# Optimization experiments

Measured on AMD Instinct MI355X. Metric: run time of the kernel, lower is better.

The kernel has to match this reference:

```python
import jax, jax.numpy as jnp
import numpy as np

B, S, P, D = 32, 512, 512, 768

def setup_inputs() -> dict:
    key = jax.random.key(0)
    k1, k2 = jax.random.split(key)
    inputs = jax.random.normal(k1, (B, S, D), dtype=jnp.float32)
    prototypes = jax.random.normal(k2, (P, D), dtype=jnp.float32)
    return {"inputs": inputs, "prototypes": prototypes}

def reference(inputs, prototypes):
    # Squared Euclidean distance from every token vector to every prototype:
    # but the cross term is a GEMM and the huge [B,S,P,D] intermediate is never built).
    x_sq = jnp.sum(inputs * inputs, axis=-1, keepdims=True)          # [B, S, 1]
    p_sq = jnp.sum(prototypes * prototypes, axis=-1)                 # [P]
    cross = jnp.einsum('bsd,pd->bsp', inputs, prototypes)            # [B, S, P]
    distances = x_sq + p_sq[None, None, :] - 2.0 * cross             # [B, S, P]
    return (distances, prototypes)
```

## Files before the change

kernel.cpp:

```cpp
#include <hip/hip_runtime.h>
#include <hip/hip_bf16.h>


#define M_TOK 16384
#define N_PROT 512
#define K_DIM 768

typedef __attribute__((ext_vector_type(4))) float f32x4;
typedef __attribute__((ext_vector_type(8))) short bf16x8;

typedef const __attribute__((address_space(1))) unsigned int g_uint;
typedef __attribute__((address_space(3))) unsigned int l_uint;

__device__ inline unsigned short f2bf(float f) {
    unsigned int u = __float_as_uint(f);
    u += 0x7fffu + ((u >> 16) & 1u);
    return (unsigned short)(u >> 16);
}

__global__ __launch_bounds__(256) void prep_kernel(
    const float* __restrict__ x, const float* __restrict__ p,
    unsigned short* __restrict__ a_bf, unsigned short* __restrict__ b_bf,
    float* __restrict__ x_sq, float* __restrict__ p_sq,
    float* __restrict__ proto_out)
{
    const int row  = blockIdx.x * 4 + (threadIdx.x >> 6);
    const int lane = threadIdx.x & 63;

    const float4* src4;
    unsigned short* dst;
    float4* pout4 = nullptr;
    if (row < M_TOK) {
        src4 = (const float4*)(x + (size_t)row * K_DIM);
        dst  = a_bf + (size_t)row * K_DIM;
    } else {
        const int r = row - M_TOK;
        src4  = (const float4*)(p + (size_t)r * K_DIM);
        dst   = b_bf + (size_t)r * K_DIM;
        pout4 = (float4*)(proto_out + (size_t)r * K_DIM);
    }

    float ssum = 0.0f;
#pragma unroll
    for (int j = 0; j < 3; ++j) {
        const int idx = lane + j * 64;
        float4 v = src4[idx];
        ssum += v.x * v.x + v.y * v.y + v.z * v.z + v.w * v.w;
        ushort4 b;
        b.x = f2bf(v.x); b.y = f2bf(v.y); b.z = f2bf(v.z); b.w = f2bf(v.w);
        ((ushort4*)dst)[idx] = b;
        if (pout4) pout4[idx] = v;
    }

#pragma unroll
    for (int off = 32; off > 0; off >>= 1) ssum += __shfl_down(ssum, off);
    if (lane == 0) {
        if (row < M_TOK) x_sq[row] = ssum;
        else             p_sq[row - M_TOK] = ssum;
    }
}

__global__ __launch_bounds__(256) void gemm_kernel(
    const unsigned short* __restrict__ A,
    const unsigned short* __restrict__ Bt,
    const float* __restrict__ x_sq, const float* __restrict__ p_sq,
    float* __restrict__ out)
{
    __shared__ unsigned short lds_a[128 * 32];
    __shared__ unsigned short lds_b[128 * 32];

    const int tid  = threadIdx.x;
    const int wave = tid >> 6;
    const int lane = tid & 63;
    const int bm = blockIdx.y << 7;
    const int bn = blockIdx.x << 7;
    const int wm = (wave >> 1) << 6;
    const int wn = (wave & 1) << 6;
    const int quad = lane >> 4;
    const int l16  = lane & 15;

    const int srow = wave * 32;
    const int lrow = lane >> 2;
    const int lcol = (lane & 3) * 8;

    const f32x4 zero = {0.0f, 0.0f, 0.0f, 0.0f};
    f32x4 acc[4][4];
#pragma unroll
    for (int mt = 0; mt < 4; ++mt)
#pragma unroll
        for (int nt = 0; nt < 4; ++nt) acc[mt][nt] = zero;

    for (int k0 = 0; k0 < K_DIM; k0 += 32) {
        __syncthreads();
#pragma unroll
        for (int i = 0; i < 2; ++i) {
            const unsigned short* ga =
                A + (size_t)(bm + srow + i * 16 + lrow) * K_DIM + k0 + lcol;
            __builtin_amdgcn_global_load_lds((g_uint*)ga,
                (l_uint*)&lds_a[(srow + i * 16) * 32], 16, 0, 0);
            const unsigned short* gb =
                Bt + (size_t)(bn + srow + i * 16 + lrow) * K_DIM + k0 + lcol;
            __builtin_amdgcn_global_load_lds((g_uint*)gb,
                (l_uint*)&lds_b[(srow + i * 16) * 32], 16, 0, 0);
        }
        __syncthreads();

        bf16x8 af[4], bfr[4];
#pragma unroll
        for (int mt = 0; mt < 4; ++mt)
            af[mt] = *(const bf16x8*)&lds_a[(wm + mt * 16 + l16) * 32 + quad * 8];
#pragma unroll
        for (int nt = 0; nt < 4; ++nt)
            bfr[nt] = *(const bf16x8*)&lds_b[(wn + nt * 16 + l16) * 32 + quad * 8];

#pragma unroll
        for (int mt = 0; mt < 4; ++mt)
#pragma unroll
            for (int nt = 0; nt < 4; ++nt)
                acc[mt][nt] = __builtin_amdgcn_mfma_f32_16x16x32_bf16(
                    af[mt], bfr[nt], acc[mt][nt], 0, 0, 0);
    }

    float ps[4];
#pragma unroll
    for (int nt = 0; nt < 4; ++nt) ps[nt] = p_sq[bn + wn + nt * 16 + l16];

#pragma unroll
    for (int mt = 0; mt < 4; ++mt) {
#pragma unroll
        for (int i = 0; i < 4; ++i) {
            const int gr = bm + wm + mt * 16 + quad * 4 + i;
            const float xs = x_sq[gr];
            float* orow = out + (size_t)gr * N_PROT + bn + wn + l16;
#pragma unroll
            for (int nt = 0; nt < 4; ++nt)
                orow[nt * 16] = xs + ps[nt] - 2.0f * acc[mt][nt][i];
        }
    }
}

extern "C" void kernel_launch(void* const* d_in, const int* in_sizes, int n_in,
                              void* d_out, int out_size, void* d_ws, size_t ws_size,
                              hipStream_t stream) {
    const float* inputs = (const float*)d_in[0];
    const float* protos = (const float*)d_in[1];
    float* out = (float*)d_out;

    char* ws = (char*)d_ws;
    unsigned short* a_bf = (unsigned short*)ws;
    unsigned short* b_bf = (unsigned short*)(ws + 25165824);
    float* x_sq = (float*)(ws + 25165824 + 786432);
    float* p_sq = (float*)(ws + 25165824 + 786432 + 65536);
    float* proto_out = out + (size_t)M_TOK * N_PROT;

    prep_kernel<<<4224, 256, 0, stream>>>(inputs, protos, a_bf, b_bf, x_sq, p_sq, proto_out);

    dim3 grid(N_PROT / 128, M_TOK / 128);
    gemm_kernel<<<grid, 256, 0, stream>>>(a_bf, b_bf, x_sq, p_sq, out);
}
```

Measured before the change: 117.1 us.

## Fuse bf16 conversion and norm computation into the GEMM kernel

Removes the separate prep kernel that converted inputs and prototypes to bf16 and computed squared norms. The GEMM kernel now loads fp32 tiles directly, computes the row norms while loading, converts to bf16 into LDS, and also writes the prototype passthrough from the first block row. The K tile grows from 32 to 64, and the launch bounds now ask for two blocks per CU. This avoids the bf16 round trip through workspace and one launch, but each block now reads fp32 data at twice the bytes. Each A tile is re-read and re-converted by the 4 column blocks, and the loads are synchronous register loads with no overlap.

```diff
diff --git a/kernel.cpp b/kernel.cpp
--- a/kernel.cpp
+++ b/kernel.cpp
@@ -5,12 +5,10 @@
 #define M_TOK 16384
 #define N_PROT 512
 #define K_DIM 768
+#define BK 64
 
 typedef __attribute__((ext_vector_type(4))) float f32x4;
 typedef __attribute__((ext_vector_type(8))) short bf16x8;
-
-typedef const __attribute__((address_space(1))) unsigned int g_uint;
-typedef __attribute__((address_space(3))) unsigned int l_uint;
 
 __device__ inline unsigned short f2bf(float f) {
     unsigned int u = __float_as_uint(f);
@@ -18,56 +16,16 @@
     return (unsigned short)(u >> 16);
 }
 
-__global__ __launch_bounds__(256) void prep_kernel(
-    const float* __restrict__ x, const float* __restrict__ p,
-    unsigned short* __restrict__ a_bf, unsigned short* __restrict__ b_bf,
-    float* __restrict__ x_sq, float* __restrict__ p_sq,
+__global__ __launch_bounds__(256, 2) void fused_dist_kernel(
+    const float* __restrict__ X,
+    const float* __restrict__ Pr,
+    float* __restrict__ out,
     float* __restrict__ proto_out)
 {
-    const int row  = blockIdx.x * 4 + (threadIdx.x >> 6);
-    const int lane = threadIdx.x & 63;
-
-    const float4* src4;
-    unsigned short* dst;
-    float4* pout4 = nullptr;
-    if (row < M_TOK) {
-        src4 = (const float4*)(x + (size_t)row * K_DIM);
-        dst  = a_bf + (size_t)row * K_DIM;
-    } else {
-        const int r = row - M_TOK;
-        src4  = (const float4*)(p + (size_t)r * K_DIM);
-        dst   = b_bf + (size_t)r * K_DIM;
-        pout4 = (float4*)(proto_out + (size_t)r * K_DIM);
-    }
-
-    float ssum = 0.0f;
-#pragma unroll
-    for (int j = 0; j < 3; ++j) {
-        const int idx = lane + j * 64;
-        float4 v = src4[idx];
-        ssum += v.x * v.x + v.y * v.y + v.z * v.z + v.w * v.w;
-        ushort4 b;
-        b.x = f2bf(v.x); b.y = f2bf(v.y); b.z = f2bf(v.z); b.w = f2bf(v.w);
-        ((ushort4*)dst)[idx] = b;
-        if (pout4) pout4[idx] = v;
-    }
-
-#pragma unroll
-    for (int off = 32; off > 0; off >>= 1) ssum += __shfl_down(ssum, off);
-    if (lane == 0) {
-        if (row < M_TOK) x_sq[row] = ssum;
-        else             p_sq[row - M_TOK] = ssum;
-    }
-}
-
-__global__ __launch_bounds__(256) void gemm_kernel(
-    const unsigned short* __restrict__ A,
-    const unsigned short* __restrict__ Bt,
-    const float* __restrict__ x_sq, const float* __restrict__ p_sq,
-    float* __restrict__ out)
-{
-    __shared__ unsigned short lds_a[128 * 32];
-    __shared__ unsigned short lds_b[128 * 32];
+    __shared__ unsigned short lds_a[128 * BK];
+    __shared__ unsigned short lds_b[128 * BK];
+    __shared__ float lds_xsq[128];
+    __shared__ float lds_psq[128];
 
     const int tid  = threadIdx.x;
     const int wave = tid >> 6;
@@ -79,9 +37,13 @@
     const int quad = lane >> 4;
     const int l16  = lane & 15;
 
-    const int srow = wave * 32;
-    const int lrow = lane >> 2;
-    const int lcol = (lane & 3) * 8;
+    const int r0 = tid >> 4;
+    const int c4 = tid & 15;
+    const bool write_proto = (blockIdx.y == 0);
+
+    float asq[8], bsq[8];
+#pragma unroll
+    for (int p = 0; p < 8; ++p) { asq[p] = 0.0f; bsq[p] = 0.0f; }
 
     const f32x4 zero = {0.0f, 0.0f, 0.0f, 0.0f};
     f32x4 acc[4][4];
@@ -90,48 +52,87 @@
 #pragma unroll
         for (int nt = 0; nt < 4; ++nt) acc[mt][nt] = zero;
 
-    for (int k0 = 0; k0 < K_DIM; k0 += 32) {
-        __syncthreads();
+    const float* Ab = X  + (size_t)(bm + r0) * K_DIM + c4 * 4;
+    const float* Bb = Pr + (size_t)(bn + r0) * K_DIM + c4 * 4;
+
+    for (int kc = 0; kc < K_DIM / BK; ++kc) {
+        const int k0 = kc * BK;
+
+        float4 av[8], bv[8];
 #pragma unroll
-        for (int i = 0; i < 2; ++i) {
-            const unsigned short* ga =
-                A + (size_t)(bm + srow + i * 16 + lrow) * K_DIM + k0 + lcol;
-            __builtin_amdgcn_global_load_lds((g_uint*)ga,
-                (l_uint*)&lds_a[(srow + i * 16) * 32], 16, 0, 0);
-            const unsigned short* gb =
-                Bt + (size_t)(bn + srow + i * 16 + lrow) * K_DIM + k0 + lcol;
-            __builtin_amdgcn_global_load_lds((g_uint*)gb,
-                (l_uint*)&lds_b[(srow + i * 16) * 32], 16, 0, 0);
+        for (int p = 0; p < 8; ++p) {
+            av[p] = *(const float4*)(Ab + (size_t)(16 * p) * K_DIM + k0);
+            bv[p] = *(const float4*)(Bb + (size_t)(16 * p) * K_DIM + k0);
         }
+
         __syncthreads();
 
-        bf16x8 af[4], bfr[4];
 #pragma unroll
-        for (int mt = 0; mt < 4; ++mt)
-            af[mt] = *(const bf16x8*)&lds_a[(wm + mt * 16 + l16) * 32 + quad * 8];
-#pragma unroll
-        for (int nt = 0; nt < 4; ++nt)
-            bfr[nt] = *(const bf16x8*)&lds_b[(wn + nt * 16 + l16) * 32 + quad * 8];
+        for (int p = 0; p < 8; ++p) {
+            asq[p] += av[p].x * av[p].x + av[p].y * av[p].y
+                    + av[p].z * av[p].z + av[p].w * av[p].w;
+            bsq[p] += bv[p].x * bv[p].x + bv[p].y * bv[p].y
+                    + bv[p].z * bv[p].z + bv[p].w * bv[p].w;
+            ushort4 ua, ub;
+            ua.x = f2bf(av[p].x); ua.y = f2bf(av[p].y);
+            ua.z = f2bf(av[p].z); ua.w = f2bf(av[p].w);
+            ub.x = f2bf(bv[p].x); ub.y = f2bf(bv[p].y);
+            ub.z = f2bf(bv[p].z); ub.w = f2bf(bv[p].w);
+            *(ushort4*)&lds_a[(r0 + 16 * p) * BK + c4 * 4] = ua;
+            *(ushort4*)&lds_b[(r0 + 16 * p) * BK + c4 * 4] = ub;
+            if (write_proto)
+                *(float4*)(proto_out + (size_t)(bn + r0 + 16 * p) * K_DIM
+                           + k0 + c4 * 4) = bv[p];
+        }
+
+        __syncthreads();
 
 #pragma unroll
-        for (int mt = 0; mt < 4; ++mt)
+        for (int ks = 0; ks < 2; ++ks) {
+            bf16x8 af[4], bfr[4];
+#pragma unroll
+            for (int mt = 0; mt < 4; ++mt)
+                af[mt] = *(const bf16x8*)
+                    &lds_a[(wm + mt * 16 + l16) * BK + ks * 32 + quad * 8];
 #pragma unroll
             for (int nt = 0; nt < 4; ++nt)
-                acc[mt][nt] = __builtin_amdgcn_mfma_f32_16x16x32_bf16(
-                    af[mt], bfr[nt], acc[mt][nt], 0, 0, 0);
+                bfr[nt] = *(const bf16x8*)
+                    &lds_b[(wn + nt * 16 + l16) * BK + ks * 32 + quad * 8];
+#pragma unroll
+            for (int mt = 0; mt < 4; ++mt)
+#pragma unroll
+                for (int nt = 0; nt < 4; ++nt)
+                    acc[mt][nt] = __builtin_amdgcn_mfma_f32_16x16x32_bf16(
+                        af[mt], bfr[nt], acc[mt][nt], 0, 0, 0);
+        }
     }
+
+#pragma unroll
+    for (int p = 0; p < 8; ++p) {
+        float a = asq[p], b = bsq[p];
+#pragma unroll
+        for (int off = 1; off < 16; off <<= 1) {
+            a += __shfl_xor(a, off);
+            b += __shfl_xor(b, off);
+        }
+        if (c4 == 0) {
+            lds_xsq[r0 + 16 * p] = a;
+            lds_psq[r0 + 16 * p] = b;
+        }
+    }
+    __syncthreads();
 
     float ps[4];
 #pragma unroll
-    for (int nt = 0; nt < 4; ++nt) ps[nt] = p_sq[bn + wn + nt * 16 + l16];
+    for (int nt = 0; nt < 4; ++nt) ps[nt] = lds_psq[wn + nt * 16 + l16];
 
 #pragma unroll
     for (int mt = 0; mt < 4; ++mt) {
 #pragma unroll
         for (int i = 0; i < 4; ++i) {
-            const int gr = bm + wm + mt * 16 + quad * 4 + i;
-            const float xs = x_sq[gr];
-            float* orow = out + (size_t)gr * N_PROT + bn + wn + l16;
+            const int lr = wm + mt * 16 + quad * 4 + i;
+            const float xs = lds_xsq[lr];
+            float* orow = out + (size_t)(bm + lr) * N_PROT + bn + wn + l16;
 #pragma unroll
             for (int nt = 0; nt < 4; ++nt)
                 orow[nt * 16] = xs + ps[nt] - 2.0f * acc[mt][nt][i];
@@ -145,16 +146,8 @@
     const float* inputs = (const float*)d_in[0];
     const float* protos = (const float*)d_in[1];
     float* out = (float*)d_out;
-
-    char* ws = (char*)d_ws;
-    unsigned short* a_bf = (unsigned short*)ws;
-    unsigned short* b_bf = (unsigned short*)(ws + 25165824);
-    float* x_sq = (float*)(ws + 25165824 + 786432);
-    float* p_sq = (float*)(ws + 25165824 + 786432 + 65536);
     float* proto_out = out + (size_t)M_TOK * N_PROT;
 
-    prep_kernel<<<4224, 256, 0, stream>>>(inputs, protos, a_bf, b_bf, x_sq, p_sq, proto_out);
-
     dim3 grid(N_PROT / 128, M_TOK / 128);
-    gemm_kernel<<<grid, 256, 0, stream>>>(a_bf, b_bf, x_sq, p_sq, out);
+    fused_dist_kernel<<<grid, 256, 0, stream>>>(inputs, protos, out, proto_out);
 }
```

After: 132.7 us. +13.3%, slower.

## Fuse fp32-to-bf16 conversion and row norms of inputs into GEMM kernel

Applied to the files above, without the earlier changes.

The prep kernel now handles only the prototypes. The main kernel reads fp32 input rows directly, converts them to bf16 into padded LDS, and accumulates x_sq on the fly. Each 512-thread block owns 64 rows and all 512 prototypes, so the A tile is read from global exactly once and the bf16 intermediate round-trip is gone. In exchange, A loads are register-staged with a simple one-step prefetch rather than direct-to-LDS, and the B chunk is reloaded per block, which raises L2 traffic on B.

```diff
diff --git a/kernel.cpp b/kernel.cpp
--- a/kernel.cpp
+++ b/kernel.cpp
@@ -5,6 +5,9 @@
 #define M_TOK 16384
 #define N_PROT 512
 #define K_DIM 768
+#define BK 32
+#define NCH (K_DIM / BK)
+#define APAD 8
 
 typedef __attribute__((ext_vector_type(4))) float f32x4;
 typedef __attribute__((ext_vector_type(8))) short bf16x8;
@@ -18,27 +21,17 @@
     return (unsigned short)(u >> 16);
 }
 
-__global__ __launch_bounds__(256) void prep_kernel(
-    const float* __restrict__ x, const float* __restrict__ p,
-    unsigned short* __restrict__ a_bf, unsigned short* __restrict__ b_bf,
-    float* __restrict__ x_sq, float* __restrict__ p_sq,
+__global__ __launch_bounds__(256) void prep_b(
+    const float* __restrict__ p,
+    unsigned short* __restrict__ b_bf, float* __restrict__ p_sq,
     float* __restrict__ proto_out)
 {
     const int row  = blockIdx.x * 4 + (threadIdx.x >> 6);
     const int lane = threadIdx.x & 63;
 
-    const float4* src4;
-    unsigned short* dst;
-    float4* pout4 = nullptr;
-    if (row < M_TOK) {
-        src4 = (const float4*)(x + (size_t)row * K_DIM);
-        dst  = a_bf + (size_t)row * K_DIM;
-    } else {
-        const int r = row - M_TOK;
-        src4  = (const float4*)(p + (size_t)r * K_DIM);
-        dst   = b_bf + (size_t)r * K_DIM;
-        pout4 = (float4*)(proto_out + (size_t)r * K_DIM);
-    }
+    const float4* src4 = (const float4*)(p + (size_t)row * K_DIM);
+    unsigned short* dst = b_bf + (size_t)row * K_DIM;
+    float4* pout4 = (float4*)(proto_out + (size_t)row * K_DIM);
 
     float ssum = 0.0f;
 #pragma unroll
@@ -49,39 +42,37 @@
         ushort4 b;
         b.x = f2bf(v.x); b.y = f2bf(v.y); b.z = f2bf(v.z); b.w = f2bf(v.w);
         ((ushort4*)dst)[idx] = b;
-        if (pout4) pout4[idx] = v;
+        pout4[idx] = v;
     }
-
 #pragma unroll
     for (int off = 32; off > 0; off >>= 1) ssum += __shfl_down(ssum, off);
-    if (lane == 0) {
-        if (row < M_TOK) x_sq[row] = ssum;
-        else             p_sq[row - M_TOK] = ssum;
-    }
+    if (lane == 0) p_sq[row] = ssum;
 }
 
-__global__ __launch_bounds__(256) void gemm_kernel(
-    const unsigned short* __restrict__ A,
-    const unsigned short* __restrict__ Bt,
-    const float* __restrict__ x_sq, const float* __restrict__ p_sq,
+__global__ __launch_bounds__(512, 2) void dist_main(
+    const float* __restrict__ X,
+    const unsigned short* __restrict__ Bb,
+    const float* __restrict__ p_sq,
     float* __restrict__ out)
 {
-    __shared__ unsigned short lds_a[128 * 32];
-    __shared__ unsigned short lds_b[128 * 32];
+    __shared__ unsigned short lds_b[N_PROT * BK];
+    __shared__ unsigned short lds_a[64 * (BK + APAD)];
+    __shared__ float lds_xsq[64];
 
     const int tid  = threadIdx.x;
     const int wave = tid >> 6;
     const int lane = tid & 63;
-    const int bm = blockIdx.y << 7;
-    const int bn = blockIdx.x << 7;
-    const int wm = (wave >> 1) << 6;
-    const int wn = (wave & 1) << 6;
+    const int bm   = blockIdx.x << 6;
+    const int wn   = wave << 6;
     const int quad = lane >> 4;
     const int l16  = lane & 15;
 
-    const int srow = wave * 32;
-    const int lrow = lane >> 2;
-    const int lcol = (lane & 3) * 8;
+    const int arow  = tid >> 3;
+    const int acol8 = tid & 7;
+    const float* aptr = X + (size_t)(bm + arow) * K_DIM + acol8 * 4;
+
+    const int brow = (lane >> 2);
+    const int bcol = (lane & 3) * 8;
 
     const f32x4 zero = {0.0f, 0.0f, 0.0f, 0.0f};
     f32x4 acc[4][4];
@@ -90,28 +81,43 @@
 #pragma unroll
         for (int nt = 0; nt < 4; ++nt) acc[mt][nt] = zero;
 
-    for (int k0 = 0; k0 < K_DIM; k0 += 32) {
+    float asq = 0.0f;
+    f32x4 cur = *(const f32x4*)aptr;
+
+    for (int kc = 0; kc < NCH; ++kc) {
+        const int k0 = kc * BK;
+
         __syncthreads();
+
 #pragma unroll
-        for (int i = 0; i < 2; ++i) {
-            const unsigned short* ga =
-                A + (size_t)(bm + srow + i * 16 + lrow) * K_DIM + k0 + lcol;
-            __builtin_amdgcn_global_load_lds((g_uint*)ga,
-                (l_uint*)&lds_a[(srow + i * 16) * 32], 16, 0, 0);
-            const unsigned short* gb =
-                Bt + (size_t)(bn + srow + i * 16 + lrow) * K_DIM + k0 + lcol;
+        for (int j = 0; j < 4; ++j) {
+            const unsigned short* gb = Bb
+                + (size_t)(wn + j * 16 + brow) * K_DIM + k0 + bcol;
             __builtin_amdgcn_global_load_lds((g_uint*)gb,
-                (l_uint*)&lds_b[(srow + i * 16) * 32], 16, 0, 0);
+                (l_uint*)&lds_b[(wn + j * 16) * BK], 16, 0, 0);
         }
+
+        f32x4 nxt = cur;
+        if (kc + 1 < NCH)
+            nxt = *(const f32x4*)(aptr + k0 + BK);
+        asq += cur.x * cur.x + cur.y * cur.y + cur.z * cur.z + cur.w * cur.w;
+        ushort4 ua;
+        ua.x = f2bf(cur.x); ua.y = f2bf(cur.y);
+        ua.z = f2bf(cur.z); ua.w = f2bf(cur.w);
+        *(ushort4*)&lds_a[arow * (BK + APAD) + acol8 * 4] = ua;
+        cur = nxt;
+
         __syncthreads();
 
         bf16x8 af[4], bfr[4];
 #pragma unroll
         for (int mt = 0; mt < 4; ++mt)
-            af[mt] = *(const bf16x8*)&lds_a[(wm + mt * 16 + l16) * 32 + quad * 8];
+            af[mt] = *(const bf16x8*)
+                &lds_a[(mt * 16 + l16) * (BK + APAD) + quad * 8];
 #pragma unroll
         for (int nt = 0; nt < 4; ++nt)
-            bfr[nt] = *(const bf16x8*)&lds_b[(wn + nt * 16 + l16) * 32 + quad * 8];
+            bfr[nt] = *(const bf16x8*)
+                &lds_b[(wn + nt * 16 + l16) * BK + quad * 8];
 
 #pragma unroll
         for (int mt = 0; mt < 4; ++mt)
@@ -121,17 +127,22 @@
                     af[mt], bfr[nt], acc[mt][nt], 0, 0, 0);
     }
 
+#pragma unroll
+    for (int off = 1; off < 8; off <<= 1) asq += __shfl_xor(asq, off);
+    if (acol8 == 0) lds_xsq[arow] = asq;
+    __syncthreads();
+
     float ps[4];
 #pragma unroll
-    for (int nt = 0; nt < 4; ++nt) ps[nt] = p_sq[bn + wn + nt * 16 + l16];
+    for (int nt = 0; nt < 4; ++nt) ps[nt] = p_sq[wn + nt * 16 + l16];
 
 #pragma unroll
     for (int mt = 0; mt < 4; ++mt) {
 #pragma unroll
         for (int i = 0; i < 4; ++i) {
-            const int gr = bm + wm + mt * 16 + quad * 4 + i;
-            const float xs = x_sq[gr];
-            float* orow = out + (size_t)gr * N_PROT + bn + wn + l16;
+            const int lr = mt * 16 + quad * 4 + i;
+            const float xs = lds_xsq[lr];
+            float* orow = out + (size_t)(bm + lr) * N_PROT + wn + l16;
 #pragma unroll
             for (int nt = 0; nt < 4; ++nt)
                 orow[nt * 16] = xs + ps[nt] - 2.0f * acc[mt][nt][i];
@@ -145,16 +156,12 @@
     const float* inputs = (const float*)d_in[0];
     const float* protos = (const float*)d_in[1];
     float* out = (float*)d_out;
+    float* proto_out = out + (size_t)M_TOK * N_PROT;
 
     char* ws = (char*)d_ws;
-    unsigned short* a_bf = (unsigned short*)ws;
-    unsigned short* b_bf = (unsigned short*)(ws + 25165824);
-    float* x_sq = (float*)(ws + 25165824 + 786432);
-    float* p_sq = (float*)(ws + 25165824 + 786432 + 65536);
-    float* proto_out = out + (size_t)M_TOK * N_PROT;
+    unsigned short* b_bf = (unsigned short*)ws;
+    float* p_sq = (float*)(ws + 786432);
 
-    prep_kernel<<<4224, 256, 0, stream>>>(inputs, protos, a_bf, b_bf, x_sq, p_sq, proto_out);
-
-    dim3 grid(N_PROT / 128, M_TOK / 128);
-    gemm_kernel<<<grid, 256, 0, stream>>>(a_bf, b_bf, x_sq, p_sq, out);
+    prep_b<<<128, 256, 0, stream>>>(protos, b_bf, p_sq, proto_out);
+    dist_main<<<M_TOK / 64, 512, 0, stream>>>(inputs, b_bf, p_sq, out);
 }
```

Result: slower. 121.8 us (+4.0%).

## Keep prototype slice resident in LDS and stream token rows from registers

Applied to the files above, without the earlier changes.

Restructures the GEMM so each 512-thread block loads a full-K 32-prototype slice into padded LDS once. Each wave then reads its token rows directly from global memory into registers with one-chunk prefetch. This removes per-iteration LDS staging and barriers for A. The trade-off is much lower reuse of the token matrix: it is re-read for every 32-column slice, which increases global/L2 traffic.

```diff
diff --git a/kernel.cpp b/kernel.cpp
--- a/kernel.cpp
+++ b/kernel.cpp
@@ -5,12 +5,12 @@
 #define M_TOK 16384
 #define N_PROT 512
 #define K_DIM 768
+#define BK 32
+#define NCH (K_DIM / BK)
+#define BSTR 40
 
 typedef __attribute__((ext_vector_type(4))) float f32x4;
 typedef __attribute__((ext_vector_type(8))) short bf16x8;
-
-typedef const __attribute__((address_space(1))) unsigned int g_uint;
-typedef __attribute__((address_space(3))) unsigned int l_uint;
 
 __device__ inline unsigned short f2bf(float f) {
     unsigned int u = __float_as_uint(f);
@@ -60,81 +60,94 @@
     }
 }
 
-__global__ __launch_bounds__(256) void gemm_kernel(
+__global__ __launch_bounds__(512, 4) void gemm_kernel(
     const unsigned short* __restrict__ A,
-    const unsigned short* __restrict__ Bt,
+    const unsigned short* __restrict__ Bb,
     const float* __restrict__ x_sq, const float* __restrict__ p_sq,
     float* __restrict__ out)
 {
-    __shared__ unsigned short lds_a[128 * 32];
-    __shared__ unsigned short lds_b[128 * 32];
+    __shared__ unsigned short lds_b[NCH * 32 * BSTR];
+    __shared__ float unused_pad;
 
     const int tid  = threadIdx.x;
     const int wave = tid >> 6;
     const int lane = tid & 63;
-    const int bm = blockIdx.y << 7;
-    const int bn = blockIdx.x << 7;
-    const int wm = (wave >> 1) << 6;
-    const int wn = (wave & 1) << 6;
+    const int bid  = blockIdx.x;
+    const int mt_  = bid & 31;
+    const int nsl  = bid >> 5;
+    const int bm   = mt_ << 9;
+    const int bn   = nsl << 5;
     const int quad = lane >> 4;
     const int l16  = lane & 15;
 
-    const int srow = wave * 32;
-    const int lrow = lane >> 2;
-    const int lcol = (lane & 3) * 8;
+    {
+        const int r  = tid >> 4;
+        const int ci = tid & 15;
+#pragma unroll
+        for (int j = 0; j < 6; ++j) {
+            const int c  = ci + 16 * j;
+            const int kc = c >> 2;
+            const int sb = c & 3;
+            bf16x8 v = *(const bf16x8*)
+                (Bb + (size_t)(bn + r) * K_DIM + kc * BK + sb * 8);
+            *(bf16x8*)&lds_b[kc * (32 * BSTR) + r * BSTR + sb * 8] = v;
+        }
+    }
+    __syncthreads();
 
     const f32x4 zero = {0.0f, 0.0f, 0.0f, 0.0f};
-    f32x4 acc[4][4];
+    f32x4 acc[4][2];
 #pragma unroll
     for (int mt = 0; mt < 4; ++mt)
 #pragma unroll
-        for (int nt = 0; nt < 4; ++nt) acc[mt][nt] = zero;
+        for (int nt = 0; nt < 2; ++nt) acc[mt][nt] = zero;
 
-    for (int k0 = 0; k0 < K_DIM; k0 += 32) {
-        __syncthreads();
+    const unsigned short* ap =
+        A + (size_t)(bm + wave * 64 + l16) * K_DIM + quad * 8;
+
+    bf16x8 acur[4], anxt[4];
 #pragma unroll
-        for (int i = 0; i < 2; ++i) {
-            const unsigned short* ga =
-                A + (size_t)(bm + srow + i * 16 + lrow) * K_DIM + k0 + lcol;
-            __builtin_amdgcn_global_load_lds((g_uint*)ga,
-                (l_uint*)&lds_a[(srow + i * 16) * 32], 16, 0, 0);
-            const unsigned short* gb =
-                Bt + (size_t)(bn + srow + i * 16 + lrow) * K_DIM + k0 + lcol;
-            __builtin_amdgcn_global_load_lds((g_uint*)gb,
-                (l_uint*)&lds_b[(srow + i * 16) * 32], 16, 0, 0);
+    for (int mt = 0; mt < 4; ++mt)
+        acur[mt] = *(const bf16x8*)(ap + (size_t)(mt * 16) * K_DIM);
+
+    for (int kc = 0; kc < NCH; ++kc) {
+        if (kc + 1 < NCH) {
+#pragma unroll
+            for (int mt = 0; mt < 4; ++mt)
+                anxt[mt] = *(const bf16x8*)
+                    (ap + (size_t)(mt * 16) * K_DIM + (kc + 1) * BK);
         }
-        __syncthreads();
 
-        bf16x8 af[4], bfr[4];
+        bf16x8 bfr[2];
 #pragma unroll
-        for (int mt = 0; mt < 4; ++mt)
-            af[mt] = *(const bf16x8*)&lds_a[(wm + mt * 16 + l16) * 32 + quad * 8];
-#pragma unroll
-        for (int nt = 0; nt < 4; ++nt)
-            bfr[nt] = *(const bf16x8*)&lds_b[(wn + nt * 16 + l16) * 32 + quad * 8];
+        for (int nt = 0; nt < 2; ++nt)
+            bfr[nt] = *(const bf16x8*)
+                &lds_b[kc * (32 * BSTR) + (nt * 16 + l16) * BSTR + quad * 8];
 
 #pragma unroll
         for (int mt = 0; mt < 4; ++mt)
 #pragma unroll
-            for (int nt = 0; nt < 4; ++nt)
+            for (int nt = 0; nt < 2; ++nt)
                 acc[mt][nt] = __builtin_amdgcn_mfma_f32_16x16x32_bf16(
-                    af[mt], bfr[nt], acc[mt][nt], 0, 0, 0);
+                    acur[mt], bfr[nt], acc[mt][nt], 0, 0, 0);
+
+#pragma unroll
+        for (int mt = 0; mt < 4; ++mt) acur[mt] = anxt[mt];
     }
 
-    float ps[4];
+    float ps[2];
 #pragma unroll
-    for (int nt = 0; nt < 4; ++nt) ps[nt] = p_sq[bn + wn + nt * 16 + l16];
+    for (int nt = 0; nt < 2; ++nt) ps[nt] = p_sq[bn + nt * 16 + l16];
 
 #pragma unroll
     for (int mt = 0; mt < 4; ++mt) {
 #pragma unroll
         for (int i = 0; i < 4; ++i) {
-            const int gr = bm + wm + mt * 16 + quad * 4 + i;
+            const int gr = bm + wave * 64 + mt * 16 + quad * 4 + i;
             const float xs = x_sq[gr];
-            float* orow = out + (size_t)gr * N_PROT + bn + wn + l16;
-#pragma unroll
-            for (int nt = 0; nt < 4; ++nt)
-                orow[nt * 16] = xs + ps[nt] - 2.0f * acc[mt][nt][i];
+            float* orow = out + (size_t)gr * N_PROT + bn + l16;
+            orow[0]  = xs + ps[0] - 2.0f * acc[mt][0][i];
+            orow[16] = xs + ps[1] - 2.0f * acc[mt][1][i];
         }
     }
 }
@@ -155,6 +168,5 @@
 
     prep_kernel<<<4224, 256, 0, stream>>>(inputs, protos, a_bf, b_bf, x_sq, p_sq, proto_out);
 
-    dim3 grid(N_PROT / 128, M_TOK / 128);
-    gemm_kernel<<<grid, 256, 0, stream>>>(a_bf, b_bf, x_sq, p_sq, out);
+    gemm_kernel<<<512, 512, 0, stream>>>(a_bf, b_bf, x_sq, p_sq, out);
 }
```

New measurement: 144.7 us. 23.6% more time.
